# Performance work log

Hardware: AMD Instinct MI355X
Metric: run time of the kernel (lower is better)

## Reference

```python
import jax, jax.numpy as jnp
import numpy as np
from jax import lax

N, D = 262144, 128
NVQ, K = 6, 512  # num_embeddings = 512 (module-level constant)


def setup_inputs() -> dict:
    key = jax.random.key(0)
    k1, k2, k3 = jax.random.split(key, 3)
    x = jax.random.normal(k1, (N, D), dtype=jnp.float32)
    codebooks = jax.random.normal(k2, (NVQ, K, D), dtype=jnp.float32)
    lin_w = jax.random.normal(k3, (D, D), dtype=jnp.float32) / np.sqrt(D)
    lin_b = jnp.zeros((D,), dtype=jnp.float32)
    return {"x": x, "codebooks": codebooks, "lin_w": lin_w, "lin_b": lin_b}


def _vq_stage(carry, E):
    # carry: (residual x [N,D], accumulated y [N,D]); E: codebook [K,D]
    x, y = carry
    d = (jnp.sum(x * x, axis=1, keepdims=True)
         - 2.0 * jnp.einsum('nd,kd->nk', x, E)
         + jnp.sum(E * E, axis=1))
    idx = jnp.argmin(d, axis=1)          # [N]
    q = E[idx]                           # gather [N, D]
    # straight-through estimator: value = q, grad flows to x
    x_hat = x + lax.stop_gradient(q - x)
    commit = jnp.mean(jnp.square(x - lax.stop_gradient(q)))
    return (x - x_hat, y + x_hat), (commit, idx)


def reference(x, codebooks, lin_w, lin_b):
    x = x.reshape(x.shape[0], D)
    y0 = jnp.zeros_like(x)
    (_, y), (commit_stage, idx_stage) = lax.scan(_vq_stage, (x, y0), codebooks)
    y = y.reshape(y.shape[0], 1, D)
    y = jnp.einsum('nsd,od->nso', y, lin_w) + lin_b  # nn.Linear(D, D)
    return y, idx_stage[0], commit_stage[0]
```

## Files before the change

### kernel.cpp

```cpp
#include <hip/hip_runtime.h>
#include <float.h>

typedef _Float16 f16;
typedef f16 f16x8 __attribute__((ext_vector_type(8)));
typedef float f32x4 __attribute__((ext_vector_type(4)));
typedef unsigned int u32;

#define NPTS 262144
#define DDIM 128
#define NVQ 6
#define KCODES 512
#define TM 64
#define BLOCKT 256

#define GLD16(gp, lp)                                                          \
    __builtin_amdgcn_global_load_lds(                                          \
        (const __attribute__((address_space(1))) void*)(gp),                   \
        (__attribute__((address_space(3))) void*)(lp), 16, 0, 0)

__device__ __forceinline__ int swz(int row, int grp) {
    return row * DDIM + ((grp ^ (row & 7)) << 3);
}
__device__ __forceinline__ u32 umin32(u32 a, u32 b) { return a < b ? a : b; }
__device__ __forceinline__ u32 umax32(u32 a, u32 b) { return a > b ? a : b; }

__device__ __forceinline__ void top2_insert(u32& k1, u32& k2, u32 key) {
    u32 ok1 = k1;
    k1 = umax32(ok1, key);
    asm("v_med3_u32 %0, %1, %2, %3" : "=v"(k2) : "v"(ok1), "v"(k2), "v"(key));
}
__device__ __forceinline__ void top2_merge(u32& k1, u32& k2, u32 o1, u32 o2) {
    u32 lo = umin32(k1, o1);
    k1 = umax32(k1, o1);
    asm("v_max3_u32 %0, %1, %2, %3" : "=v"(k2) : "v"(k2), "v"(o2), "v"(lo));
}

__device__ __forceinline__ f16x8 cvt8(float4 a, float4 b) {
    f16x8 h;
    h[0] = (f16)a.x; h[1] = (f16)a.y; h[2] = (f16)a.z; h[3] = (f16)a.w;
    h[4] = (f16)b.x; h[5] = (f16)b.y; h[6] = (f16)b.z; h[7] = (f16)b.w;
    return h;
}

__global__ void zero_commit_kernel(float* p) { *p = 0.0f; }

__global__ void norms_kernel(const float* __restrict__ cb, float* __restrict__ norms,
                             float* __restrict__ ascore) {
    int row = blockIdx.x;
    int lane = threadIdx.x;
    const float* r = cb + (size_t)row * DDIM;
    float2 v = *(const float2*)(r + lane * 2);
    float s = v.x * v.x + v.y * v.y;
    #pragma unroll
    for (int m = 32; m >= 1; m >>= 1) s += __shfl_xor(s, m);
    if (lane == 0) { norms[row] = s; ascore[row] = 512.0f - 0.5f * s; }
}

__global__ void preconv_kernel(const float* __restrict__ cb, f16* __restrict__ cb16) {
    size_t base = ((size_t)blockIdx.x * 256 + threadIdx.x) * 8;
    float4 a = *(const float4*)(cb + base);
    float4 b = *(const float4*)(cb + base + 4);
    *(f16x8*)(cb16 + base) = cvt8(a, b);
}

template<bool PRE>
__global__ __launch_bounds__(BLOCKT)
__attribute__((amdgpu_waves_per_eu(4, 4)))
void rvq_kernel(const float* __restrict__ x, const float* __restrict__ cb,
                const f16* __restrict__ cb16, const float* __restrict__ W,
                const float* __restrict__ bias, const float* __restrict__ norms,
                const float* __restrict__ ascore, float* __restrict__ out) {
    __shared__ f16   rh[TM * DDIM];
    __shared__ f16   ebuf[4][2048];
    __shared__ float as_lds[KCODES];
    __shared__ uint2 cand[4][TM];

    const int tid  = threadIdx.x;
    const int wid  = tid >> 6;
    const int lane = tid & 63;
    const int g    = lane >> 4;
    const int li   = lane & 15;
    const int p_own = tid >> 2;
    const int q     = tid & 3;
    const int p0    = blockIdx.x * TM;

    const int srow = (lane >> 4);
    const int sgrp = lane & 15;

    float r[32];
    {
        const float* xs = x + (size_t)(p0 + p_own) * DDIM + q * 32;
        #pragma unroll
        for (int k = 0; k < 8; ++k) {
            float4 v = *(const float4*)(xs + 4 * k);
            r[4*k] = v.x; r[4*k+1] = v.y; r[4*k+2] = v.z; r[4*k+3] = v.w;
        }
    }
    #pragma unroll
    for (int k = 0; k < 4; ++k) {
        f16x8 h;
        #pragma unroll
        for (int m = 0; m < 8; ++m) h[m] = (f16)r[8*k+m];
        *(f16x8*)&rh[swz(p_own, q * 4 + k)] = h;
    }

    as_lds[tid]       = ascore[tid];
    as_lds[tid + 256] = ascore[tid + 256];
    if constexpr (PRE) {
        const char* gsb0 = (const char*)cb16 + ((size_t)16 * wid) * (DDIM * 2);
        char* lb = (char*)&ebuf[wid][0];
        #pragma unroll
        for (int it = 0; it < 4; ++it) {
            int row = it * 4 + srow;
            GLD16(gsb0 + row * 256 + ((sgrp ^ (row & 7)) << 4), lb + it * 1024);
        }
    }
    __syncthreads();

    float commit_part = 0.0f;

    #pragma unroll 1
    for (int s = 0; s < NVQ; ++s) {
        u32 k1[4], k2[4];
        #pragma unroll
        for (int j = 0; j < 4; ++j) { k1[j] = 0u; k2[j] = 0u; }

        if constexpr (PRE) {
            const char* gsb = (const char*)cb16 +
                              ((size_t)s * KCODES + 16 * wid) * (DDIM * 2);
            char* lb = (char*)&ebuf[wid][0];

            #pragma unroll 1
            for (int ch = 0; ch < 8; ++ch) {
                asm volatile("s_waitcnt vmcnt(0)" ::: "memory");

                float4 as4 = *(const float4*)&as_lds[ch * 64 + 16 * wid + 4 * g];
                f32x4 ainit;
                ainit[0] = as4.x; ainit[1] = as4.y; ainit[2] = as4.z; ainit[3] = as4.w;
                f32x4 acc[4];
                #pragma unroll
                for (int j = 0; j < 4; ++j) acc[j] = ainit;

                __builtin_amdgcn_s_setprio(1);
                #pragma unroll
                for (int ks = 0; ks < 4; ++ks) {
                    f16x8 Af = *(const f16x8*)(lb + li * 256 +
                                               (((ks * 4 + g) ^ (li & 7)) << 4));
                    #pragma unroll
                    for (int j = 0; j < 4; ++j) {
                        f16x8 Bf = *(const f16x8*)&rh[swz(16 * j + li, ks * 4 + g)];
                        acc[j] = __builtin_amdgcn_mfma_f32_16x16x32_f16(Af, Bf, acc[j], 0, 0, 0);
                    }
                }
                __builtin_amdgcn_s_setprio(0);

                asm volatile("s_waitcnt lgkmcnt(0)" ::: "memory");
                if (ch < 7) {
                    #pragma unroll
                    for (int it = 0; it < 4; ++it) {
                        int row = it * 4 + srow;
                        GLD16(gsb + (size_t)(ch + 1) * 16384 + row * 256 +
                                  ((sgrp ^ (row & 7)) << 4),
                              lb + it * 1024);
                    }
                } else if (s < NVQ - 1) {
                    const char* gsbn = gsb + (size_t)KCODES * DDIM * 2;
                    #pragma unroll
                    for (int it = 0; it < 4; ++it) {
                        int row = it * 4 + srow;
                        GLD16(gsbn + row * 256 + ((sgrp ^ (row & 7)) << 4),
                              lb + it * 1024);
                    }
                }

                const int invc = 511 - (ch * 64 + 16 * wid + 4 * g);
                #pragma unroll
                for (int j = 0; j < 4; ++j) {
                    #pragma unroll
                    for (int reg = 0; reg < 4; ++reg) {
                        u32 key = (__float_as_uint(acc[j][reg]) & 0xFFFFFE00u) |
                                  (u32)(invc - reg);
                        top2_insert(k1[j], k2[j], key);
                    }
                }
            }
        } else {
            f16x8 Bf[4][4];
            #pragma unroll
            for (int j = 0; j < 4; ++j)
                #pragma unroll
                for (int ks = 0; ks < 4; ++ks)
                    Bf[j][ks] = *(const f16x8*)&rh[swz(16 * j + li, ks * 4 + g)];
            const float* Ab32 = cb + ((size_t)s * KCODES + 16 * wid + li) * DDIM + g * 8;
            #pragma unroll 2
            for (int ch = 0; ch < 8; ++ch) {
                float4 as4 = *(const float4*)&as_lds[ch * 64 + 16 * wid + 4 * g];
                f32x4 ainit;
                ainit[0] = as4.x; ainit[1] = as4.y; ainit[2] = as4.z; ainit[3] = as4.w;
                f32x4 acc[4];
                #pragma unroll
                for (int j = 0; j < 4; ++j) acc[j] = ainit;
                #pragma unroll
                for (int ks = 0; ks < 4; ++ks) {
                    const float* ap = Ab32 + (size_t)ch * 64 * DDIM + ks * 32;
                    f16x8 Af = cvt8(*(const float4*)ap, *(const float4*)(ap + 4));
                    #pragma unroll
                    for (int j = 0; j < 4; ++j)
                        acc[j] = __builtin_amdgcn_mfma_f32_16x16x32_f16(Af, Bf[j][ks], acc[j], 0, 0, 0);
                }
                const int invc = 511 - (ch * 64 + 16 * wid + 4 * g);
                #pragma unroll
                for (int j = 0; j < 4; ++j) {
                    #pragma unroll
                    for (int reg = 0; reg < 4; ++reg) {
                        u32 key = (__float_as_uint(acc[j][reg]) & 0xFFFFFE00u) |
                                  (u32)(invc - reg);
                        top2_insert(k1[j], k2[j], key);
                    }
                }
            }
        }

        #pragma unroll
        for (int m = 16; m <= 32; m <<= 1) {
            #pragma unroll
            for (int j = 0; j < 4; ++j) {
                u32 o1 = (u32)__shfl_xor((int)k1[j], m);
                u32 o2 = (u32)__shfl_xor((int)k2[j], m);
                top2_merge(k1[j], k2[j], o1, o2);
            }
        }
        if (lane < 16) {
            #pragma unroll
            for (int j = 0; j < 4; ++j)
                cand[wid][16 * j + li] = make_uint2(k1[j], k2[j]);
        }
        __syncthreads();

        float as_n0 = 0.0f, as_n1 = 0.0f;
        if (s < NVQ - 1) {
            as_n0 = ascore[(s + 1) * KCODES + tid];
            as_n1 = ascore[(s + 1) * KCODES + tid + 256];
        }

        uint2 v0 = cand[0][p_own];
        u32 m1 = v0.x, m2 = v0.y;
        #pragma unroll
        for (int w = 1; w < 4; ++w) {
            uint2 vv = cand[w][p_own];
            top2_merge(m1, m2, vv.x, vv.y);
        }
        int c1 = 511 - (int)(m1 & 0x1FFu);
        int c2 = 511 - (int)(m2 & 0x1FFu);

        const float* E1 = cb + (size_t)(s * KCODES + c1) * DDIM + q * 32;
        const float* E2 = cb + (size_t)(s * KCODES + c2) * DDIM + q * 32;
        float dot1 = 0.0f, dot2 = 0.0f;
        #pragma unroll
        for (int k = 0; k < 8; ++k) {
            float4 a = *(const float4*)(E1 + 4 * k);
            dot1 += a.x * r[4*k] + a.y * r[4*k+1] + a.z * r[4*k+2] + a.w * r[4*k+3];
        }
        #pragma unroll
        for (int k = 0; k < 8; ++k) {
            float4 a = *(const float4*)(E2 + 4 * k);
            dot2 += a.x * r[4*k] + a.y * r[4*k+1] + a.z * r[4*k+2] + a.w * r[4*k+3];
        }
        dot1 += __shfl_xor(dot1, 1); dot1 += __shfl_xor(dot1, 2);
        dot2 += __shfl_xor(dot2, 1); dot2 += __shfl_xor(dot2, 2);
        float d1e = fmaf(-2.0f, dot1, norms[s * KCODES + c1]);
        float d2e = fmaf(-2.0f, dot2, norms[s * KCODES + c2]);
        int best = (d2e < d1e || (d2e == d1e && c2 < c1)) ? c2 : c1;

        if (s == 0 && q == 0)
            out[(size_t)NPTS * DDIM + p0 + p_own] = (float)best;

        {
            const float* Eb = cb + (size_t)(s * KCODES + best) * DDIM + q * 32;
            float cp = 0.0f;
            #pragma unroll
            for (int k = 0; k < 8; ++k) {
                float4 e = *(const float4*)(Eb + 4 * k);
                r[4*k]   -= e.x; r[4*k+1] -= e.y; r[4*k+2] -= e.z; r[4*k+3] -= e.w;
                cp += r[4*k]*r[4*k] + r[4*k+1]*r[4*k+1] + r[4*k+2]*r[4*k+2] + r[4*k+3]*r[4*k+3];
            }
            if (s == 0) commit_part = cp;
        }
        if (s < NVQ - 1) {
            #pragma unroll
            for (int k = 0; k < 4; ++k) {
                f16x8 h;
                #pragma unroll
                for (int m = 0; m < 8; ++m) h[m] = (f16)r[8*k+m];
                *(f16x8*)&rh[swz(p_own, q * 4 + k)] = h;
            }
            as_lds[tid]       = as_n0;
            as_lds[tid + 256] = as_n1;
        }
        __syncthreads();
    }

    {
        const float* xs = x + (size_t)(p0 + p_own) * DDIM + q * 32;
        #pragma unroll
        for (int k = 0; k < 4; ++k) {
            float4 a = *(const float4*)(xs + 8 * k);
            float4 b = *(const float4*)(xs + 8 * k + 4);
            f16x8 h;
            h[0]=(f16)(a.x - r[8*k+0]); h[1]=(f16)(a.y - r[8*k+1]);
            h[2]=(f16)(a.z - r[8*k+2]); h[3]=(f16)(a.w - r[8*k+3]);
            h[4]=(f16)(b.x - r[8*k+4]); h[5]=(f16)(b.y - r[8*k+5]);
            h[6]=(f16)(b.z - r[8*k+6]); h[7]=(f16)(b.w - r[8*k+7]);
            *(f16x8*)&rh[swz(p_own, q * 4 + k)] = h;
        }
    }
    __syncthreads();

    {
        f16x8 Yf[4][4];
        #pragma unroll
        for (int j = 0; j < 4; ++j)
            #pragma unroll
            for (int ks = 0; ks < 4; ++ks)
                Yf[j][ks] = *(const f16x8*)&rh[swz(16 * j + li, ks * 4 + g)];

        #pragma unroll 1
        for (int ch = 0; ch < 2; ++ch) {
            float4 b4 = *(const float4*)(bias + ch * 64 + 16 * wid + 4 * g);
            f32x4 acc[4];
            #pragma unroll
            for (int j = 0; j < 4; ++j) {
                acc[j][0] = b4.x; acc[j][1] = b4.y; acc[j][2] = b4.z; acc[j][3] = b4.w;
            }
            __builtin_amdgcn_s_setprio(1);
            #pragma unroll
            for (int ks = 0; ks < 4; ++ks) {
                const float* wp = W + (size_t)(ch * 64 + 16 * wid + li) * DDIM + ks * 32 + g * 8;
                f16x8 Af = cvt8(*(const float4*)wp, *(const float4*)(wp + 4));
                #pragma unroll
                for (int j = 0; j < 4; ++j)
                    acc[j] = __builtin_amdgcn_mfma_f32_16x16x32_f16(Af, Yf[j][ks], acc[j], 0, 0, 0);
            }
            __builtin_amdgcn_s_setprio(0);
            int obase = ch * 64 + 16 * wid + 4 * g;
            #pragma unroll
            for (int j = 0; j < 4; ++j)
                *(float4*)(out + (size_t)(p0 + 16 * j + li) * DDIM + obase) =
                    make_float4(acc[j][0], acc[j][1], acc[j][2], acc[j][3]);
        }
    }

    {
        float cp = commit_part;
        #pragma unroll
        for (int m = 1; m <= 32; m <<= 1) cp += __shfl_xor(cp, m);
        __syncthreads();
        float* wsum = (float*)cand;
        if (lane == 0) wsum[wid] = cp;
        __syncthreads();
        if (tid == 0) {
            float t = (wsum[0] + wsum[1]) + (wsum[2] + wsum[3]);
            atomicAdd(out + (size_t)NPTS * DDIM + NPTS,
                      t * (1.0f / ((float)NPTS * (float)DDIM)));
        }
    }
}

extern "C" void kernel_launch(void* const* d_in, const int* in_sizes, int n_in,
                              void* d_out, int out_size, void* d_ws, size_t ws_size,
                              hipStream_t stream) {
    const float* x    = (const float*)d_in[0];
    const float* cb   = (const float*)d_in[1];
    const float* linw = (const float*)d_in[2];
    const float* linb = (const float*)d_in[3];
    float* out    = (float*)d_out;
    float* norms  = (float*)d_ws;
    float* ascore = norms + 4096;
    f16*   cb16   = (f16*)((char*)d_ws + 32768);
    const size_t need = 32768 + (size_t)NVQ * KCODES * DDIM * 2;

    zero_commit_kernel<<<1, 1, 0, stream>>>(out + (size_t)NPTS * DDIM + NPTS);
    norms_kernel<<<NVQ * KCODES, 64, 0, stream>>>(cb, norms, ascore);

    if (ws_size >= need) {
        preconv_kernel<<<(NVQ * KCODES * DDIM) / (256 * 8), 256, 0, stream>>>(cb, cb16);
        rvq_kernel<true><<<NPTS / TM, BLOCKT, 0, stream>>>(x, cb, cb16, linw, linb,
                                                           norms, ascore, out);
    } else {
        rvq_kernel<false><<<NPTS / TM, BLOCKT, 0, stream>>>(x, cb, cb16, linw, linb,
                                                            norms, ascore, out);
    }
}
```

Baseline: 548.8 us.

## Split per-wave codebook staging into two K-halves for finer-grained load overlap

Each wave's 16-row codebook chunk in LDS is split into two halves along the D dimension (new layout with 128-byte rows per half). The MFMA loop processes the first half, then issues the next chunk's load for that half while computing on the second half, with vmcnt(2) waits instead of vmcnt(0). This is meant to hide global-to-LDS latency behind MFMA work inside the single buffer. It adds more waits and changes the swizzle layout, which risks bank conflicts or ordering mistakes.

New measurement: 508.3 us. 7.4% less time.

```diff
diff --git a/kernel.cpp b/kernel.cpp
--- a/kernel.cpp
+++ b/kernel.cpp
@@ -40,6 +40,15 @@
     h[0] = (f16)a.x; h[1] = (f16)a.y; h[2] = (f16)a.z; h[3] = (f16)a.w;
     h[4] = (f16)b.x; h[5] = (f16)b.y; h[6] = (f16)b.z; h[7] = (f16)b.w;
     return h;
+}
+
+__device__ __forceinline__ void stage_half(const char* gbase, int h, char* dst, int lane) {
+    #pragma unroll
+    for (int it2 = 0; it2 < 2; ++it2) {
+        int row = it2 * 8 + (lane >> 3);
+        int hg  = lane & 7;
+        GLD16(gbase + row * 256 + ((h * 8 + (hg ^ (row & 7))) << 4), dst + it2 * 1024);
+    }
 }
 
 __global__ void zero_commit_kernel(float* p) { *p = 0.0f; }
@@ -84,9 +93,6 @@
     const int q     = tid & 3;
     const int p0    = blockIdx.x * TM;
 
-    const int srow = (lane >> 4);
-    const int sgrp = lane & 15;
-
     float r[32];
     {
         const float* xs = x + (size_t)(p0 + p_own) * DDIM + q * 32;
@@ -109,11 +115,8 @@
     if constexpr (PRE) {
         const char* gsb0 = (const char*)cb16 + ((size_t)16 * wid) * (DDIM * 2);
         char* lb = (char*)&ebuf[wid][0];
-        #pragma unroll
-        for (int it = 0; it < 4; ++it) {
-            int row = it * 4 + srow;
-            GLD16(gsb0 + row * 256 + ((sgrp ^ (row & 7)) << 4), lb + it * 1024);
-        }
+        stage_half(gsb0, 0, lb, lane);
+        stage_half(gsb0, 1, lb + 2048, lane);
     }
     __syncthreads();
 
@@ -128,11 +131,12 @@
         if constexpr (PRE) {
             const char* gsb = (const char*)cb16 +
                               ((size_t)s * KCODES + 16 * wid) * (DDIM * 2);
+            const char* gsbn = gsb + (size_t)KCODES * DDIM * 2;
             char* lb = (char*)&ebuf[wid][0];
 
             #pragma unroll 1
             for (int ch = 0; ch < 8; ++ch) {
-                asm volatile("s_waitcnt vmcnt(0)" ::: "memory");
+                asm volatile("s_waitcnt vmcnt(2)" ::: "memory");
 
                 float4 as4 = *(const float4*)&as_lds[ch * 64 + 16 * wid + 4 * g];
                 f32x4 ainit;
@@ -143,8 +147,8 @@
 
                 __builtin_amdgcn_s_setprio(1);
                 #pragma unroll
-                for (int ks = 0; ks < 4; ++ks) {
-                    f16x8 Af = *(const f16x8*)(lb + li * 256 +
+                for (int ks = 0; ks < 2; ++ks) {
+                    f16x8 Af = *(const f16x8*)(lb + li * 128 +
                                                (((ks * 4 + g) ^ (li & 7)) << 4));
                     #pragma unroll
                     for (int j = 0; j < 4; ++j) {
@@ -153,25 +157,30 @@
                     }
                 }
                 __builtin_amdgcn_s_setprio(0);
-
                 asm volatile("s_waitcnt lgkmcnt(0)" ::: "memory");
-                if (ch < 7) {
+                if (ch < 7)            stage_half(gsb + (size_t)(ch + 1) * 16384, 0, lb, lane);
+                else if (s < NVQ - 1)  stage_half(gsbn, 0, lb, lane);
+
+                if (ch == 7 && s == NVQ - 1)
+                    asm volatile("s_waitcnt vmcnt(0)" ::: "memory");
+                else
+                    asm volatile("s_waitcnt vmcnt(2)" ::: "memory");
+
+                __builtin_amdgcn_s_setprio(1);
+                #pragma unroll
+                for (int ks = 2; ks < 4; ++ks) {
+                    f16x8 Af = *(const f16x8*)(lb + 2048 + li * 128 +
+                                               ((((ks - 2) * 4 + g) ^ (li & 7)) << 4));
                     #pragma unroll
-                    for (int it = 0; it < 4; ++it) {
-                        int row = it * 4 + srow;
-                        GLD16(gsb + (size_t)(ch + 1) * 16384 + row * 256 +
-                                  ((sgrp ^ (row & 7)) << 4),
-                              lb + it * 1024);
-                    }
-                } else if (s < NVQ - 1) {
-                    const char* gsbn = gsb + (size_t)KCODES * DDIM * 2;
-                    #pragma unroll
-                    for (int it = 0; it < 4; ++it) {
-                        int row = it * 4 + srow;
-                        GLD16(gsbn + row * 256 + ((sgrp ^ (row & 7)) << 4),
-                              lb + it * 1024);
+                    for (int j = 0; j < 4; ++j) {
+                        f16x8 Bf = *(const f16x8*)&rh[swz(16 * j + li, ks * 4 + g)];
+                        acc[j] = __builtin_amdgcn_mfma_f32_16x16x32_f16(Af, Bf, acc[j], 0, 0, 0);
                     }
                 }
+                __builtin_amdgcn_s_setprio(0);
+                asm volatile("s_waitcnt lgkmcnt(0)" ::: "memory");
+                if (ch < 7)            stage_half(gsb + (size_t)(ch + 1) * 16384, 1, lb + 2048, lane);
+                else if (s < NVQ - 1)  stage_half(gsbn, 1, lb + 2048, lane);
 
                 const int invc = 511 - (ch * 64 + 16 * wid + 4 * g);
                 #pragma unroll
```
